# Kernel optimization log

Hardware: AMD Instinct MI355X
Metric: run time of the kernel (lower is better)

The kernel has to match this reference:

```python
import jax, jax.numpy as jnp
import numpy as np

EPS = 1e-16


def setup_inputs() -> dict:
    key = jax.random.key(0)
    ks = jax.random.split(key, 7)
    B, N, C = 4096, 2048, 128  # batch of heads, memory rows, memory cols
    k = jax.random.normal(ks[0], (B, C), dtype=jnp.float32)
    beta = jax.random.normal(ks[1], (B, 1), dtype=jnp.float32)
    g = jax.random.normal(ks[2], (B, 1), dtype=jnp.float32)
    s = jax.random.normal(ks[3], (B, 3), dtype=jnp.float32)
    gamma = jax.random.normal(ks[4], (B, 1), dtype=jnp.float32)
    w_prev = jax.random.uniform(ks[5], (B, N), dtype=jnp.float32)
    w_prev = w_prev / jnp.sum(w_prev, axis=1, keepdims=True)  # valid weighting
    M = jax.random.normal(ks[6], (N, C), dtype=jnp.float32)  # memory matrix
    return {"k": k, "beta": beta, "g": g, "s": s, "gamma": gamma,
            "w_prev": w_prev, "M": M}


def reference(k, beta, g, s, gamma, w_prev, M):
    # head activations
    beta = jax.nn.softplus(beta)            # [B,1] key strength > 0
    g = jax.nn.sigmoid(g)                   # [B,1] interpolation gate
    s = jax.nn.softmax(s, axis=-1)          # [B,3] shift distribution
    gamma = 1.0 + jax.nn.softplus(gamma)    # [B,1] sharpening >= 1

    # content addressing: cosine similarity k vs memory rows
    k_norm = jnp.linalg.norm(k, axis=-1, keepdims=True)          # [B,1]
    m_norm = jnp.linalg.norm(M, axis=-1, keepdims=True)          # [N,1]
    sim = jnp.einsum('bc,nc->bn', k, M) / (k_norm * m_norm.T + EPS)  # [B,N]
    w_c = jax.nn.softmax(beta * sim, axis=-1)                    # [B,N]

    # interpolation with previous weighting
    w_g = g * w_c + (1.0 - g) * w_prev                           # [B,N]

    # circular convolution with 3-tap shift kernel (shifts -1, 0, +1)
    w_tilde = (s[:, 0:1] * jnp.roll(w_g, 1, axis=1)
               + s[:, 1:2] * w_g
               + s[:, 2:3] * jnp.roll(w_g, -1, axis=1))          # [B,N]

    # sharpening
    w_sharp = w_tilde ** gamma
    w = w_sharp / (jnp.sum(w_sharp, axis=1, keepdims=True) + EPS)
    return w
```

## Files before the change

kernel.cpp:

```cpp
#include <hip/hip_runtime.h>
#include <math.h>

#define NN 2048
#define CC 128
#define ROWS 16
#define EPSF 1e-16f

typedef __attribute__((ext_vector_type(8))) short bf16x8;
typedef __attribute__((ext_vector_type(4))) float f32x4;

__device__ __forceinline__ float softplusf(float x) {
  return fmaxf(x, 0.0f) + log1pf(__expf(-fabsf(x)));
}

union U8 { uint u[4]; bf16x8 v; };

__device__ __forceinline__ void split8(float4 a, float4 b, bf16x8& hi,
                                       bf16x8& lo, float& sq) {
  float f[8] = {a.x, a.y, a.z, a.w, b.x, b.y, b.z, b.w};
  U8 H, L;
#pragma unroll
  for (int i = 0; i < 4; ++i) {
    float f0 = f[2 * i], f1 = f[2 * i + 1];
    sq += f0 * f0;
    sq += f1 * f1;
    uint u0 = __float_as_uint(f0), u1 = __float_as_uint(f1);
    uint m0 = u0 & 0xffff0000u, m1 = u1 & 0xffff0000u;
    float r0 = f0 - __uint_as_float(m0);
    float r1 = f1 - __uint_as_float(m1);
    H.u[i] = (u0 >> 16) | m1;
    L.u[i] = (__float_as_uint(r0) >> 16) | (__float_as_uint(r1) & 0xffff0000u);
  }
  hi = H.v;
  lo = L.v;
}

__global__ __launch_bounds__(256) void ntm_prep_kernel(
    const float* __restrict__ kptr, const float* __restrict__ beta_,
    const float* __restrict__ g_, const float* __restrict__ s_,
    const float* __restrict__ gamma_, const float* __restrict__ M,
    bf16x8* __restrict__ Mhf, bf16x8* __restrict__ Mlf,
    bf16x8* __restrict__ Khf, bf16x8* __restrict__ Klf,
    float* __restrict__ imn, float* __restrict__ zb, float* __restrict__ gvv,
    float* __restrict__ gmv, float* __restrict__ s0a, float* __restrict__ s1a,
    float* __restrict__ s2a) {
  const int bid = blockIdx.x;
  const int t = threadIdx.x;
  if (bid < 96) {
    const int lane = t & 63;
    const int wv = t >> 6;
    const int l15 = lane & 15;
    const int lg = lane >> 4;
    const bool isM = bid < 32;
    const int grp = (isM ? bid : bid - 32) * 4 + wv;
    const float* src = (isM ? M : kptr) + (grp * 16 + l15) * CC + lg * 8;
    bf16x8* dh = (isM ? Mhf : Khf) + (grp * 4) * 64 + lane;
    bf16x8* dl = (isM ? Mlf : Klf) + (grp * 4) * 64 + lane;
    float sq = 0.f;
#pragma unroll
    for (int ks = 0; ks < 4; ++ks) {
      float4 a0 = *(const float4*)(src + ks * 32);
      float4 a1 = *(const float4*)(src + ks * 32 + 4);
      bf16x8 h, l;
      split8(a0, a1, h, l, sq);
      dh[ks * 64] = h;
      dl[ks * 64] = l;
    }
    sq += __shfl_xor(sq, 16, 64);
    sq += __shfl_xor(sq, 32, 64);
    if (lg == 0) {
      const int row = grp * 16 + l15;
      if (isM) {
        imn[row] = 1.0f / sqrtf(sq);
      } else {
        zb[row] = softplusf(beta_[row]) / sqrtf(sq);
      }
    }
  } else {
    const int r = (bid - 96) * 256 + t;
    gvv[r] = 1.0f / (1.0f + __expf(-g_[r]));
    gmv[r] = 1.0f + softplusf(gamma_[r]);
    float sh0 = s_[3 * r], sh1 = s_[3 * r + 1], sh2 = s_[3 * r + 2];
    float shm = fmaxf(sh0, fmaxf(sh1, sh2));
    float e0 = __expf(sh0 - shm), e1 = __expf(sh1 - shm), e2 = __expf(sh2 - shm);
    float sden = 1.0f / (e0 + e1 + e2);
    s0a[r] = e0 * sden;
    s1a[r] = e1 * sden;
    s2a[r] = e2 * sden;
  }
}

__global__ __launch_bounds__(1024) void ntm_main_kernel(
    const float* __restrict__ w_prev, const bf16x8* __restrict__ Mhf,
    const bf16x8* __restrict__ Mlf, const bf16x8* __restrict__ Khf,
    const bf16x8* __restrict__ Klf, const float* __restrict__ imn,
    const float* __restrict__ zb, const float* __restrict__ gvv,
    const float* __restrict__ gmv, const float* __restrict__ s0a,
    const float* __restrict__ s1a, const float* __restrict__ s2a,
    float* __restrict__ out) {
  __shared__ float red[ROWS][16];
  __shared__ float edges[ROWS][16][2];

  const int t = threadIdx.x;
  const int lane = t & 63;
  const int w = __builtin_amdgcn_readfirstlane(t >> 6);
  const int l15 = lane & 15;
  const int lg = lane >> 4;
  const int bg = blockIdx.x;
  const int b0 = bg * ROWS;

  f32x4 accT[8];
#pragma unroll
  for (int tt = 0; tt < 8; ++tt) accT[tt] = (f32x4){0.f, 0.f, 0.f, 0.f};

#pragma unroll
  for (int ks = 0; ks < 4; ++ks) {
    bf16x8 bh[8], bl[8];
#pragma unroll
    for (int tt = 0; tt < 8; ++tt) {
      const int gM = 8 * w + tt;
      bh[tt] = Mhf[(gM * 4 + ks) * 64 + lane];
      bl[tt] = Mlf[(gM * 4 + ks) * 64 + lane];
    }
    const bf16x8 ah = Khf[(bg * 4 + ks) * 64 + lane];
    const bf16x8 al = Klf[(bg * 4 + ks) * 64 + lane];
#pragma unroll
    for (int tt = 0; tt < 8; ++tt) {
      accT[tt] = __builtin_amdgcn_mfma_f32_16x16x32_bf16(ah, bh[tt], accT[tt], 0, 0, 0);
      accT[tt] = __builtin_amdgcn_mfma_f32_16x16x32_bf16(al, bh[tt], accT[tt], 0, 0, 0);
      accT[tt] = __builtin_amdgcn_mfma_f32_16x16x32_bf16(ah, bl[tt], accT[tt], 0, 0, 0);
    }
  }

  float wp[4][8];
#pragma unroll
  for (int q = 0; q < 4; ++q) {
    const size_t rbase = (size_t)(b0 + lg * 4 + q) * NN + 128 * w + l15;
#pragma unroll
    for (int tt = 0; tt < 8; ++tt) wp[q][tt] = w_prev[rbase + 16 * tt];
  }
  float imn_t[8];
#pragma unroll
  for (int tt = 0; tt < 8; ++tt) imn_t[tt] = imn[128 * w + 16 * tt + l15];
  float zbv[4], gvq[4];
#pragma unroll
  for (int q = 0; q < 4; ++q) {
    zbv[q] = zb[b0 + lg * 4 + q];
    gvq[q] = gvv[b0 + lg * 4 + q];
  }

#pragma unroll
  for (int q = 0; q < 4; ++q) {
    const int rr = lg * 4 + q;
    float rs = 0.f;
#pragma unroll
    for (int tt = 0; tt < 8; ++tt) {
      float e = __expf(accT[tt][q] * imn_t[tt] * zbv[q]);
      accT[tt][q] = e;
      rs += e;
    }
    rs += __shfl_xor(rs, 1, 64);
    rs += __shfl_xor(rs, 2, 64);
    rs += __shfl_xor(rs, 4, 64);
    rs += __shfl_xor(rs, 8, 64);
    if (l15 == 0) red[rr][w] = rs;
  }
  __syncthreads();

#pragma unroll
  for (int q = 0; q < 4; ++q) {
    const int rr = lg * 4 + q;
    float4 p0 = *(const float4*)&red[rr][0];
    float4 p1 = *(const float4*)&red[rr][4];
    float4 p2 = *(const float4*)&red[rr][8];
    float4 p3 = *(const float4*)&red[rr][12];
    float tot = (p0.x + p0.y + p0.z + p0.w) + (p1.x + p1.y + p1.z + p1.w) +
                (p2.x + p2.y + p2.z + p2.w) + (p3.x + p3.y + p3.z + p3.w);
    const float gv = gvq[q];
    const float ge = gv / tot;
    const float om = 1.0f - gv;
#pragma unroll
    for (int tt = 0; tt < 8; ++tt) {
      accT[tt][q] = ge * accT[tt][q] + om * wp[q][tt];
    }
    if (l15 == 0) edges[rr][w][0] = accT[0][q];
    if (l15 == 15) edges[rr][w][1] = accT[7][q];
  }
  __syncthreads();

  const int tm = (lane & 48) | ((lane + 15) & 15);
  const int tp = (lane & 48) | ((lane + 1) & 15);
#pragma unroll
  for (int q = 0; q < 4; ++q) {
    const int rr = lg * 4 + q;
    const float sh0 = s0a[b0 + rr];
    const float sh1 = s1a[b0 + rr];
    const float sh2 = s2a[b0 + rr];
    const float gammav = gmv[b0 + rr];
    const float eL = edges[rr][(w + 15) & 15][1];
    const float eR = edges[rr][(w + 1) & 15][0];

    float sm[8], sp[8];
#pragma unroll
    for (int tt = 0; tt < 8; ++tt) {
      sm[tt] = __shfl(accT[tt][q], tm, 64);
      sp[tt] = __shfl(accT[tt][q], tp, 64);
    }
    float rs = 0.f;
#pragma unroll
    for (int tt = 0; tt < 8; ++tt) {
      float pv = (l15 == 0) ? ((tt == 0) ? eL : sm[tt - 1]) : sm[tt];
      float nx = (l15 == 15) ? ((tt == 7) ? eR : sp[tt + 1]) : sp[tt];
      float wt = sh0 * pv + sh1 * accT[tt][q] + sh2 * nx;
      float p = __expf(gammav * __logf(wt));
      accT[tt][q] = p;
      rs += p;
    }
    rs += __shfl_xor(rs, 1, 64);
    rs += __shfl_xor(rs, 2, 64);
    rs += __shfl_xor(rs, 4, 64);
    rs += __shfl_xor(rs, 8, 64);
    if (l15 == 0) red[rr][w] = rs;
  }
  __syncthreads();

#pragma unroll
  for (int q = 0; q < 4; ++q) {
    const int rr = lg * 4 + q;
    float4 p0 = *(const float4*)&red[rr][0];
    float4 p1 = *(const float4*)&red[rr][4];
    float4 p2 = *(const float4*)&red[rr][8];
    float4 p3 = *(const float4*)&red[rr][12];
    float tot = (p0.x + p0.y + p0.z + p0.w) + (p1.x + p1.y + p1.z + p1.w) +
                (p2.x + p2.y + p2.z + p2.w) + (p3.x + p3.y + p3.z + p3.w);
    const float pinv = 1.0f / (tot + EPSF);
    const size_t rbase = (size_t)(b0 + rr) * NN + 128 * w + l15;
#pragma unroll
    for (int tt = 0; tt < 8; ++tt) {
      out[rbase + 16 * tt] = accT[tt][q] * pinv;
    }
  }
}

__global__ __launch_bounds__(1024) void ntm_main_fallback(
    const float* __restrict__ kptr, const float* __restrict__ beta_,
    const float* __restrict__ g_, const float* __restrict__ s_,
    const float* __restrict__ gamma_, const float* __restrict__ w_prev,
    const float* __restrict__ Mptr, float* __restrict__ out) {
  __shared__ float red[ROWS][16];
  __shared__ float edges[ROWS][16][2];
  const int t = threadIdx.x;
  const int lane = t & 63;
  const int w = __builtin_amdgcn_readfirstlane(t >> 6);
  const int l15 = lane & 15;
  const int lg = lane >> 4;
  const int b0 = blockIdx.x * ROWS;

  const float* kr = kptr + (b0 + l15) * CC + lg * 8;
  bf16x8 ah[4], al[4];
  float ksq = 0.f;
#pragma unroll
  for (int ks = 0; ks < 4; ++ks) {
    float4 a0 = *(const float4*)(kr + ks * 32);
    float4 a1 = *(const float4*)(kr + ks * 32 + 4);
    split8(a0, a1, ah[ks], al[ks], ksq);
  }
  ksq += __shfl_xor(ksq, 16, 64);
  ksq += __shfl_xor(ksq, 32, 64);
  const float ikn_own = 1.0f / sqrtf(ksq);

  f32x4 accT[8];
  float imn[8];
#pragma unroll
  for (int tt = 0; tt < 8; ++tt) {
    const int n0t = 128 * w + 16 * tt;
    const float* mr = Mptr + (size_t)(n0t + l15) * CC + lg * 8;
    f32x4 acc = {0.f, 0.f, 0.f, 0.f};
    float msq = 0.f;
#pragma unroll
    for (int ks = 0; ks < 4; ++ks) {
      float4 m0 = *(const float4*)(mr + ks * 32);
      float4 m1 = *(const float4*)(mr + ks * 32 + 4);
      bf16x8 bh, bl;
      split8(m0, m1, bh, bl, msq);
      acc = __builtin_amdgcn_mfma_f32_16x16x32_bf16(ah[ks], bh, acc, 0, 0, 0);
      acc = __builtin_amdgcn_mfma_f32_16x16x32_bf16(al[ks], bh, acc, 0, 0, 0);
      acc = __builtin_amdgcn_mfma_f32_16x16x32_bf16(ah[ks], bl, acc, 0, 0, 0);
    }
    msq += __shfl_xor(msq, 16, 64);
    msq += __shfl_xor(msq, 32, 64);
    imn[tt] = 1.0f / sqrtf(msq);
    accT[tt] = acc;
  }

#pragma unroll
  for (int q = 0; q < 4; ++q) {
    const int rr = lg * 4 + q;
    const float zb = softplusf(beta_[b0 + rr]) * __shfl(ikn_own, rr, 64);
    float rs = 0.f;
#pragma unroll
    for (int tt = 0; tt < 8; ++tt) {
      float e = __expf(accT[tt][q] * imn[tt] * zb);
      accT[tt][q] = e;
      rs += e;
    }
    rs += __shfl_xor(rs, 1, 64);
    rs += __shfl_xor(rs, 2, 64);
    rs += __shfl_xor(rs, 4, 64);
    rs += __shfl_xor(rs, 8, 64);
    if (l15 == 0) red[rr][w] = rs;
  }
  __syncthreads();

#pragma unroll
  for (int q = 0; q < 4; ++q) {
    const int rr = lg * 4 + q;
    float4 p0 = *(const float4*)&red[rr][0];
    float4 p1 = *(const float4*)&red[rr][4];
    float4 p2 = *(const float4*)&red[rr][8];
    float4 p3 = *(const float4*)&red[rr][12];
    float tot = (p0.x + p0.y + p0.z + p0.w) + (p1.x + p1.y + p1.z + p1.w) +
                (p2.x + p2.y + p2.z + p2.w) + (p3.x + p3.y + p3.z + p3.w);
    const float gv = 1.0f / (1.0f + __expf(-g_[b0 + rr]));
    const float ge = gv / tot;
    const float om = 1.0f - gv;
    const size_t rbase = (size_t)(b0 + rr) * NN + 128 * w + l15;
#pragma unroll
    for (int tt = 0; tt < 8; ++tt) {
      float wpv = w_prev[rbase + 16 * tt];
      accT[tt][q] = ge * accT[tt][q] + om * wpv;
    }
    if (l15 == 0) edges[rr][w][0] = accT[0][q];
    if (l15 == 15) edges[rr][w][1] = accT[7][q];
  }
  __syncthreads();

  const int tm = (lane & 48) | ((lane + 15) & 15);
  const int tp = (lane & 48) | ((lane + 1) & 15);
#pragma unroll
  for (int q = 0; q < 4; ++q) {
    const int rr = lg * 4 + q;
    float sh0 = s_[3 * (b0 + rr)];
    float sh1 = s_[3 * (b0 + rr) + 1];
    float sh2 = s_[3 * (b0 + rr) + 2];
    float shm = fmaxf(sh0, fmaxf(sh1, sh2));
    float e0 = __expf(sh0 - shm), e1 = __expf(sh1 - shm), e2 = __expf(sh2 - shm);
    float sden = 1.0f / (e0 + e1 + e2);
    sh0 = e0 * sden; sh1 = e1 * sden; sh2 = e2 * sden;
    const float gammav = 1.0f + softplusf(gamma_[b0 + rr]);
    const float eL = edges[rr][(w + 15) & 15][1];
    const float eR = edges[rr][(w + 1) & 15][0];
    float sm[8], sp[8];
#pragma unroll
    for (int tt = 0; tt < 8; ++tt) {
      sm[tt] = __shfl(accT[tt][q], tm, 64);
      sp[tt] = __shfl(accT[tt][q], tp, 64);
    }
    float rs = 0.f;
#pragma unroll
    for (int tt = 0; tt < 8; ++tt) {
      float pv = (l15 == 0) ? ((tt == 0) ? eL : sm[tt - 1]) : sm[tt];
      float nx = (l15 == 15) ? ((tt == 7) ? eR : sp[tt + 1]) : sp[tt];
      float wt = sh0 * pv + sh1 * accT[tt][q] + sh2 * nx;
      float p = __expf(gammav * __logf(wt));
      accT[tt][q] = p;
      rs += p;
    }
    rs += __shfl_xor(rs, 1, 64);
    rs += __shfl_xor(rs, 2, 64);
    rs += __shfl_xor(rs, 4, 64);
    rs += __shfl_xor(rs, 8, 64);
    if (l15 == 0) red[rr][w] = rs;
  }
  __syncthreads();

#pragma unroll
  for (int q = 0; q < 4; ++q) {
    const int rr = lg * 4 + q;
    float4 p0 = *(const float4*)&red[rr][0];
    float4 p1 = *(const float4*)&red[rr][4];
    float4 p2 = *(const float4*)&red[rr][8];
    float4 p3 = *(const float4*)&red[rr][12];
    float tot = (p0.x + p0.y + p0.z + p0.w) + (p1.x + p1.y + p1.z + p1.w) +
                (p2.x + p2.y + p2.z + p2.w) + (p3.x + p3.y + p3.z + p3.w);
    const float pinv = 1.0f / (tot + EPSF);
    const size_t rbase = (size_t)(b0 + rr) * NN + 128 * w + l15;
#pragma unroll
    for (int tt = 0; tt < 8; ++tt) {
      out[rbase + 16 * tt] = accT[tt][q] * pinv;
    }
  }
}

extern "C" void kernel_launch(void* const* d_in, const int* in_sizes, int n_in,
                              void* d_out, int out_size, void* d_ws, size_t ws_size,
                              hipStream_t stream) {
  const float* k = (const float*)d_in[0];
  const float* beta = (const float*)d_in[1];
  const float* g = (const float*)d_in[2];
  const float* s = (const float*)d_in[3];
  const float* gamma = (const float*)d_in[4];
  const float* w_prev = (const float*)d_in[5];
  const float* M = (const float*)d_in[6];
  float* out = (float*)d_out;

  char* ws = (char*)d_ws;
  bf16x8* Mhf = (bf16x8*)(ws + 0);
  bf16x8* Mlf = (bf16x8*)(ws + 524288);
  bf16x8* Khf = (bf16x8*)(ws + 1048576);
  bf16x8* Klf = (bf16x8*)(ws + 2097152);
  float* imn = (float*)(ws + 3145728);
  float* zb = imn + 2048;
  float* gvv = zb + 4096;
  float* gmv = gvv + 4096;
  float* s0a = gmv + 4096;
  float* s1a = s0a + 4096;
  float* s2a = s1a + 4096;
  const size_t need = 3145728 + 2048 * 4 + 6 * 4096 * 4;

  if (ws_size >= need) {
    ntm_prep_kernel<<<112, 256, 0, stream>>>(k, beta, g, s, gamma, M, Mhf, Mlf,
                                             Khf, Klf, imn, zb, gvv, gmv, s0a,
                                             s1a, s2a);
    ntm_main_kernel<<<4096 / ROWS, 1024, 0, stream>>>(
        w_prev, Mhf, Mlf, Khf, Klf, imn, zb, gvv, gmv, s0a, s1a, s2a, out);
  } else {
    ntm_main_fallback<<<4096 / ROWS, 1024, 0, stream>>>(k, beta, g, s, gamma,
                                                        w_prev, M, out);
  }
}
```

Before: 42.59 us.

## Permute memory-row packing so each lane owns 8 contiguous columns

The prep kernel now packs M rows in a permuted order so that, in the main kernel, each lane's 8 MFMA output tiles map to 8 consecutive memory columns instead of columns strided by 16. This lets w_prev, the inverse norms and the output be read and written with float4 vector accesses rather than scalar strided ones. The circular shift now needs only two cross-lane shuffles per row instead of sixteen. The K fragments are also hoisted out of the k-loop. The permutation must stay consistent between prep, the MFMA B operand, imn indexing and the edge handling.

```diff
diff --git a/kernel.cpp b/kernel.cpp
--- a/kernel.cpp
+++ b/kernel.cpp
@@ -3,7 +3,6 @@
 
 #define NN 2048
 #define CC 128
-#define ROWS 16
 #define EPSF 1e-16f
 
 typedef __attribute__((ext_vector_type(8))) short bf16x8;
@@ -53,7 +52,9 @@
     const int lg = lane >> 4;
     const bool isM = bid < 32;
     const int grp = (isM ? bid : bid - 32) * 4 + wv;
-    const float* src = (isM ? M : kptr) + (grp * 16 + l15) * CC + lg * 8;
+    const int nrow = isM ? ((grp >> 3) * 128 + 8 * l15 + (grp & 7))
+                         : (grp * 16 + l15);
+    const float* src = (isM ? M : kptr) + nrow * CC + lg * 8;
     bf16x8* dh = (isM ? Mhf : Khf) + (grp * 4) * 64 + lane;
     bf16x8* dl = (isM ? Mlf : Klf) + (grp * 4) * 64 + lane;
     float sq = 0.f;
@@ -69,11 +70,10 @@
     sq += __shfl_xor(sq, 16, 64);
     sq += __shfl_xor(sq, 32, 64);
     if (lg == 0) {
-      const int row = grp * 16 + l15;
       if (isM) {
-        imn[row] = 1.0f / sqrtf(sq);
+        imn[nrow] = 1.0f / sqrtf(sq);
       } else {
-        zb[row] = softplusf(beta_[row]) / sqrtf(sq);
+        zb[nrow] = softplusf(beta_[nrow]) / sqrtf(sq);
       }
     }
   } else {
@@ -98,8 +98,8 @@
     const float* __restrict__ gmv, const float* __restrict__ s0a,
     const float* __restrict__ s1a, const float* __restrict__ s2a,
     float* __restrict__ out) {
-  __shared__ float red[ROWS][16];
-  __shared__ float edges[ROWS][16][2];
+  __shared__ float red[16][16];
+  __shared__ float edges[16][16][2];
 
   const int t = threadIdx.x;
   const int lane = t & 63;
@@ -107,7 +107,14 @@
   const int l15 = lane & 15;
   const int lg = lane >> 4;
   const int bg = blockIdx.x;
-  const int b0 = bg * ROWS;
+  const int b0 = bg * 16;
+
+  bf16x8 ah[4], al[4];
+#pragma unroll
+  for (int ks = 0; ks < 4; ++ks) {
+    ah[ks] = Khf[(bg * 4 + ks) * 64 + lane];
+    al[ks] = Klf[(bg * 4 + ks) * 64 + lane];
+  }
 
   f32x4 accT[8];
 #pragma unroll
@@ -122,31 +129,32 @@
       bh[tt] = Mhf[(gM * 4 + ks) * 64 + lane];
       bl[tt] = Mlf[(gM * 4 + ks) * 64 + lane];
     }
-    const bf16x8 ah = Khf[(bg * 4 + ks) * 64 + lane];
-    const bf16x8 al = Klf[(bg * 4 + ks) * 64 + lane];
-#pragma unroll
-    for (int tt = 0; tt < 8; ++tt) {
-      accT[tt] = __builtin_amdgcn_mfma_f32_16x16x32_bf16(ah, bh[tt], accT[tt], 0, 0, 0);
-      accT[tt] = __builtin_amdgcn_mfma_f32_16x16x32_bf16(al, bh[tt], accT[tt], 0, 0, 0);
-      accT[tt] = __builtin_amdgcn_mfma_f32_16x16x32_bf16(ah, bl[tt], accT[tt], 0, 0, 0);
-    }
-  }
-
+#pragma unroll
+    for (int tt = 0; tt < 8; ++tt) {
+      accT[tt] = __builtin_amdgcn_mfma_f32_16x16x32_bf16(ah[ks], bh[tt], accT[tt], 0, 0, 0);
+      accT[tt] = __builtin_amdgcn_mfma_f32_16x16x32_bf16(al[ks], bh[tt], accT[tt], 0, 0, 0);
+      accT[tt] = __builtin_amdgcn_mfma_f32_16x16x32_bf16(ah[ks], bl[tt], accT[tt], 0, 0, 0);
+    }
+  }
+
+  const int ncol0 = 128 * w + 8 * l15;
+  const float4 i0 = *(const float4*)&imn[ncol0];
+  const float4 i1 = *(const float4*)&imn[ncol0 + 4];
+  float imn_t[8] = {i0.x, i0.y, i0.z, i0.w, i1.x, i1.y, i1.z, i1.w};
+
+  const float4* w_prev4 = (const float4*)w_prev;
   float wp[4][8];
-#pragma unroll
-  for (int q = 0; q < 4; ++q) {
-    const size_t rbase = (size_t)(b0 + lg * 4 + q) * NN + 128 * w + l15;
-#pragma unroll
-    for (int tt = 0; tt < 8; ++tt) wp[q][tt] = w_prev[rbase + 16 * tt];
-  }
-  float imn_t[8];
-#pragma unroll
-  for (int tt = 0; tt < 8; ++tt) imn_t[tt] = imn[128 * w + 16 * tt + l15];
   float zbv[4], gvq[4];
 #pragma unroll
   for (int q = 0; q < 4; ++q) {
-    zbv[q] = zb[b0 + lg * 4 + q];
-    gvq[q] = gvv[b0 + lg * 4 + q];
+    const int rr = lg * 4 + q;
+    const size_t r4 = (size_t)(b0 + rr) * (NN / 4) + (ncol0 >> 2);
+    float4 wa = w_prev4[r4];
+    float4 wb = w_prev4[r4 + 1];
+    wp[q][0] = wa.x; wp[q][1] = wa.y; wp[q][2] = wa.z; wp[q][3] = wa.w;
+    wp[q][4] = wb.x; wp[q][5] = wb.y; wp[q][6] = wb.z; wp[q][7] = wb.w;
+    zbv[q] = zb[b0 + rr];
+    gvq[q] = gvv[b0 + rr];
   }
 
 #pragma unroll
@@ -200,18 +208,18 @@
     const float eL = edges[rr][(w + 15) & 15][1];
     const float eR = edges[rr][(w + 1) & 15][0];
 
-    float sm[8], sp[8];
-#pragma unroll
-    for (int tt = 0; tt < 8; ++tt) {
-      sm[tt] = __shfl(accT[tt][q], tm, 64);
-      sp[tt] = __shfl(accT[tt][q], tp, 64);
-    }
+    float wg[8];
+#pragma unroll
+    for (int tt = 0; tt < 8; ++tt) wg[tt] = accT[tt][q];
+    const float pmv = __shfl(wg[7], tm, 64);
+    const float npv = __shfl(wg[0], tp, 64);
+
     float rs = 0.f;
 #pragma unroll
     for (int tt = 0; tt < 8; ++tt) {
-      float pv = (l15 == 0) ? ((tt == 0) ? eL : sm[tt - 1]) : sm[tt];
-      float nx = (l15 == 15) ? ((tt == 7) ? eR : sp[tt + 1]) : sp[tt];
-      float wt = sh0 * pv + sh1 * accT[tt][q] + sh2 * nx;
+      float pv = (tt == 0) ? ((l15 == 0) ? eL : pmv) : wg[tt - 1];
+      float nx = (tt == 7) ? ((l15 == 15) ? eR : npv) : wg[tt + 1];
+      float wt = sh0 * pv + sh1 * wg[tt] + sh2 * nx;
       float p = __expf(gammav * __logf(wt));
       accT[tt][q] = p;
       rs += p;
@@ -224,6 +232,7 @@
   }
   __syncthreads();
 
+  float4* out4 = (float4*)out;
 #pragma unroll
   for (int q = 0; q < 4; ++q) {
     const int rr = lg * 4 + q;
@@ -234,11 +243,14 @@
     float tot = (p0.x + p0.y + p0.z + p0.w) + (p1.x + p1.y + p1.z + p1.w) +
                 (p2.x + p2.y + p2.z + p2.w) + (p3.x + p3.y + p3.z + p3.w);
     const float pinv = 1.0f / (tot + EPSF);
-    const size_t rbase = (size_t)(b0 + rr) * NN + 128 * w + l15;
-#pragma unroll
-    for (int tt = 0; tt < 8; ++tt) {
-      out[rbase + 16 * tt] = accT[tt][q] * pinv;
-    }
+    const size_t r4 = (size_t)(b0 + rr) * (NN / 4) + (ncol0 >> 2);
+    float4 o0, o1;
+    o0.x = accT[0][q] * pinv; o0.y = accT[1][q] * pinv;
+    o0.z = accT[2][q] * pinv; o0.w = accT[3][q] * pinv;
+    o1.x = accT[4][q] * pinv; o1.y = accT[5][q] * pinv;
+    o1.z = accT[6][q] * pinv; o1.w = accT[7][q] * pinv;
+    out4[r4] = o0;
+    out4[r4 + 1] = o1;
   }
 }
 
@@ -247,14 +259,14 @@
     const float* __restrict__ g_, const float* __restrict__ s_,
     const float* __restrict__ gamma_, const float* __restrict__ w_prev,
     const float* __restrict__ Mptr, float* __restrict__ out) {
-  __shared__ float red[ROWS][16];
-  __shared__ float edges[ROWS][16][2];
+  __shared__ float red[16][16];
+  __shared__ float edges[16][16][2];
   const int t = threadIdx.x;
   const int lane = t & 63;
   const int w = __builtin_amdgcn_readfirstlane(t >> 6);
   const int l15 = lane & 15;
   const int lg = lane >> 4;
-  const int b0 = blockIdx.x * ROWS;
+  const int b0 = blockIdx.x * 16;
 
   const float* kr = kptr + (b0 + l15) * CC + lg * 8;
   bf16x8 ah[4], al[4];
@@ -422,10 +434,10 @@
     ntm_prep_kernel<<<112, 256, 0, stream>>>(k, beta, g, s, gamma, M, Mhf, Mlf,
                                              Khf, Klf, imn, zb, gvv, gmv, s0a,
                                              s1a, s2a);
-    ntm_main_kernel<<<4096 / ROWS, 1024, 0, stream>>>(
-        w_prev, Mhf, Mlf, Khf, Klf, imn, zb, gvv, gmv, s0a, s1a, s2a, out);
+    ntm_main_kernel<<<256, 1024, 0, stream>>>(w_prev, Mhf, Mlf, Khf, Klf, imn,
+                                              zb, gvv, gmv, s0a, s1a, s2a, out);
   } else {
-    ntm_main_fallback<<<4096 / ROWS, 1024, 0, stream>>>(k, beta, g, s, gamma,
-                                                        w_prev, M, out);
-  }
-}
+    ntm_main_fallback<<<256, 1024, 0, stream>>>(k, beta, g, s, gamma, w_prev,
+                                                M, out);
+  }
+}
```

After: 45.39 us. +6.6%, slower.
